# Kernel optimization log

Hardware: AMD Instinct MI355X
Metric: run time of the kernel (lower is better)

The kernel has to match this reference:

```python
import jax, jax.numpy as jnp
import numpy as np

R, C, N, E, H, F, ED, G, L = 1, 4, 50000, 200000, 128, 128, 16, 64, 2


def setup_inputs() -> dict:
    key = jax.random.key(0)
    ks = jax.random.split(key, 16)
    s = 0.05
    return {
        "x": jax.random.normal(ks[0], (R * C * N, H), jnp.float32),
        "batch": jnp.sort(jax.random.randint(ks[1], (N,), 0, G)),
        "edge_index": jax.random.randint(ks[2], (2, E), 0, N),
        "edge_attr": jax.random.normal(ks[3], (1, 1, E, ED), jnp.float32),
        "node_mask": jax.random.uniform(ks[4], (R, C, N, 1), jnp.float32),
        "edge_mask": jax.random.uniform(ks[5], (R, C, E, 1), jnp.float32),
        "W_be": jax.random.normal(ks[6], (ED, H), jnp.float32) * s,
        "b_be": jnp.zeros((H,), jnp.float32),
        "eps": jnp.zeros((L,), jnp.float32),
        "W1": jax.random.normal(ks[7], (L, H, H), jnp.float32) * s,
        "b1": jnp.zeros((L, H), jnp.float32),
        "W2": jax.random.normal(ks[8], (L, H, H), jnp.float32) * s,
        "b2": jnp.zeros((L, H), jnp.float32),
        "Wm1": jax.random.normal(ks[9], (H, H), jnp.float32) * s,
        "bm1": jnp.zeros((H,), jnp.float32),
        "Wm2": jax.random.normal(ks[10], (H, F), jnp.float32) * s,
        "bm2": jnp.zeros((F,), jnp.float32),
    }


def reference(x, batch, edge_index, edge_attr, node_mask, edge_mask,
              W_be, b_be, eps, W1, b1, W2, b2, Wm1, bm1, Wm2, bm2):
    gelu = lambda v: jax.nn.gelu(v, approximate=False)  # torch F.gelu default is erf
    src, dst = edge_index[0], edge_index[1]
    # bond encoder, shared across conv layers: (1,1,E,H)
    ee = edge_attr @ W_be + b_be
    for l in range(L):
        ux = x.reshape(R, C, N, H)
        # gather + add + GELU + edge-weight multiply: (R,C,E,H)
        msg = gelu(ux[:, :, src, :] + ee) * edge_mask
        # scatter_sum over edges into destination nodes
        agg = jnp.zeros_like(ux).at[:, :, dst, :].add(msg)
        h = (1.0 + eps[l]) * x + agg.reshape(x.shape)
        # conv MLP: Linear -> GELU -> Linear, then outer GELU (norm=Identity, dropout=0)
        h = gelu(h @ W1[l] + b1[l]) @ W2[l] + b2[l]
        x = gelu(h)
    # final node MLP (PyG MLP, norm=None): Linear -> GELU -> Linear
    x = gelu(x @ Wm1 + bm1) @ Wm2 + bm2  # (R*C*N, F)
    x4 = x.reshape(R, C, N, F)
    # masked mean-pool per (repeat, centroid, graph)
    num = jnp.zeros((R, C, G, F), x.dtype).at[:, :, batch, :].add(x4 * node_mask)
    den = jnp.zeros((R, C, G, 1), x.dtype).at[:, :, batch, :].add(node_mask) + 1e-7
    pooled = (num / den).transpose(0, 2, 1, 3).reshape(-1, F)  # (R*G*C, F)
    return pooled
```

## Files before the change

kernel.cpp:

```cpp
#include <hip/hip_runtime.h>
#include <math.h>

#define NN 50000
#define EN 200000
#define CC 4
#define HH 128
#define GG 64
#define LDSA 136
#define LDSF 132

typedef __attribute__((ext_vector_type(8))) short bs8;
typedef __attribute__((ext_vector_type(4))) float f32x4;
typedef __attribute__((ext_vector_type(2))) float f32x2;

__device__ __forceinline__ unsigned short f2bf(float f) {
  unsigned int u = __float_as_uint(f);
  u += 0x7FFFu + ((u >> 16) & 1u);
  return (unsigned short)(u >> 16);
}
__device__ __forceinline__ float bf2f(unsigned short h) {
  return __uint_as_float(((unsigned int)h) << 16);
}
__device__ __forceinline__ float gelu_f(float x) {
  float z = fabsf(x) * 0.7071067811865476f;
  float t = __builtin_amdgcn_rcpf(fmaf(0.3275911f, z, 1.0f));
  float poly = t * fmaf(t, fmaf(t, fmaf(t, fmaf(t, 1.061405429f, -1.453152027f),
                                        1.421413741f), -0.284496736f), 0.254829592f);
  float e = fmaf(-poly, __expf(-z * z), 1.0f);
  return 0.5f * x * (1.0f + copysignf(e, x));
}
__device__ __forceinline__ float gelu2_f(float x) {
  float z = fabsf(x) * 0.7071067811865476f;
  float t = __builtin_amdgcn_rcpf(fmaf(0.3275911f, z, 1.0f));
  float poly = t * fmaf(t, fmaf(t, fmaf(t, fmaf(t, 1.061405429f, -1.453152027f),
                                        1.421413741f), -0.284496736f), 0.254829592f);
  float e = fmaf(-poly, __expf(-z * z), 1.0f);
  return x * (1.0f + copysignf(e, x));
}

__global__ __launch_bounds__(256) void count_kernel(const int* __restrict__ dst,
                                                    int* __restrict__ counts) {
  int e = blockIdx.x * 256 + threadIdx.x;
  if (e < EN) atomicAdd(&counts[dst[e]], 1);
}

__global__ __launch_bounds__(256) void block_sum_kernel(const int* __restrict__ counts,
                                                        int* __restrict__ bsums) {
  int tid = threadIdx.x;
  int i = blockIdx.x * 256 + tid;
  int v = (i < NN) ? counts[i] : 0;
#pragma unroll
  for (int d = 1; d < 64; d <<= 1) v += __shfl_xor(v, d);
  __shared__ int ws4[4];
  if ((tid & 63) == 0) ws4[tid >> 6] = v;
  __syncthreads();
  if (tid == 0) bsums[blockIdx.x] = ws4[0] + ws4[1] + ws4[2] + ws4[3];
}

__global__ __launch_bounds__(256) void bsum_scan_kernel(const int* __restrict__ bsums,
                                                        int* __restrict__ boffs, int nb) {
  int tid = threadIdx.x, lane = tid & 63, wv = tid >> 6;
  int v = (tid < nb) ? bsums[tid] : 0;
  int s = v;
#pragma unroll
  for (int d = 1; d < 64; d <<= 1) { int t = __shfl_up(s, d); if (lane >= d) s += t; }
  __shared__ int wsum[4];
  if (lane == 63) wsum[wv] = s;
  __syncthreads();
  int pre = 0;
  for (int j = 0; j < wv; ++j) pre += wsum[j];
  if (tid < nb) boffs[tid] = pre + s - v;
}

__global__ __launch_bounds__(256) void block_scan_kernel(const int* __restrict__ counts,
                                                         const int* __restrict__ boffs,
                                                         int* __restrict__ offsets,
                                                         int* __restrict__ cursor) {
  int tid = threadIdx.x, lane = tid & 63, wv = tid >> 6;
  int i = blockIdx.x * 256 + tid;
  int v = (i < NN) ? counts[i] : 0;
  int s = v;
#pragma unroll
  for (int d = 1; d < 64; d <<= 1) { int t = __shfl_up(s, d); if (lane >= d) s += t; }
  __shared__ int wsum[4];
  if (lane == 63) wsum[wv] = s;
  __syncthreads();
  int pre = boffs[blockIdx.x];
  for (int j = 0; j < wv; ++j) pre += wsum[j];
  if (i < NN) { int e = pre + s - v; offsets[i] = e; cursor[i] = e; }
  if (i == 0) offsets[NN] = EN;
}

__global__ __launch_bounds__(256) void fill_kernel(const int* __restrict__ dst,
                                                   const int* __restrict__ src,
                                                   const float* __restrict__ emask,
                                                   int* __restrict__ cursor,
                                                   int2* __restrict__ csr_es,
                                                   float4* __restrict__ emask_s) {
  int e = blockIdx.x * 256 + threadIdx.x;
  if (e < EN) {
    int s = src[e];
    float m0 = emask[e];
    float m1 = emask[EN + e];
    float m2 = emask[2 * EN + e];
    float m3 = emask[3 * EN + e];
    int pos = atomicAdd(&cursor[dst[e]], 1);
    csr_es[pos] = make_int2(e, s);
    emask_s[pos] = make_float4(m0, m1, m2, m3);
  }
}

__global__ __launch_bounds__(256) void prep_w_kernel(const float* __restrict__ W1,
                                                     const float* __restrict__ W2,
                                                     const float* __restrict__ Wm1,
                                                     const float* __restrict__ Wm2,
                                                     unsigned short* __restrict__ wts) {
  int m = blockIdx.x >> 6;
  int idx = (blockIdx.x & 63) * 256 + threadIdx.x;
  const float* src = (m == 0) ? W1 : (m == 1) ? W1 + 16384 : (m == 2) ? W2
                     : (m == 3) ? W2 + 16384 : (m == 4) ? Wm1 : Wm2;
  unsigned short* dhi = wts + m * 32768;
  unsigned short* dlo = dhi + 16384;
  int n = idx >> 7, k = idx & 127;
  float v = src[k * HH + n];
  unsigned short hi = f2bf(v);
  dhi[n * HH + k] = hi;
  dlo[n * HH + k] = f2bf(v - bf2f(hi));
}

__global__ __launch_bounds__(256) void ee_kernel(const float* __restrict__ eattr,
                                                 const float* __restrict__ Wbe,
                                                 const float* __restrict__ bbe,
                                                 float* __restrict__ ee) {
  __shared__ float Ws[16 * HH];
  __shared__ float Ea[16 * 16];
  int tid = threadIdx.x;
  int e0 = blockIdx.x * 16;
#pragma unroll
  for (int i = 0; i < 8; ++i) Ws[tid + i * 256] = Wbe[tid + i * 256];
  Ea[tid] = eattr[(size_t)e0 * 16 + tid];
  __syncthreads();
  int h = tid & 127, half = tid >> 7;
  float bb = bbe[h];
#pragma unroll
  for (int j = 0; j < 8; ++j) {
    int el = j * 2 + half;
    float acc = bb;
#pragma unroll
    for (int d = 0; d < 16; ++d) acc += Ea[el * 16 + d] * Ws[d * HH + h];
    ee[(size_t)(e0 + el) * HH + h] = acc;
  }
}

__device__ __forceinline__ void loadW(const unsigned short* __restrict__ whi,
                                      const unsigned short* __restrict__ wlo,
                                      bs8 (&bh)[4][2], bs8 (&bl)[4][2],
                                      int ln, int quad, int wq) {
#pragma unroll
  for (int ks = 0; ks < 4; ++ks)
#pragma unroll
    for (int nt = 0; nt < 2; ++nt) {
      int wrow = ((wq * 2 + nt) * 16 + ln) * HH + ks * 32 + quad * 8;
      bh[ks][nt] = *(const bs8*)(whi + wrow);
      bl[ks][nt] = *(const bs8*)(wlo + wrow);
    }
}
__device__ __forceinline__ void zacc(f32x4 (&acc)[4][2]) {
#pragma unroll
  for (int mt = 0; mt < 4; ++mt)
#pragma unroll
    for (int nt = 0; nt < 2; ++nt)
#pragma unroll
      for (int r = 0; r < 4; ++r) acc[mt][nt][r] = 0.f;
}
__device__ __forceinline__ void gemm3(const unsigned short* Ahi, const unsigned short* Alo,
                                      const bs8 (&bh)[4][2], const bs8 (&bl)[4][2],
                                      f32x4 (&acc)[4][2], int ln, int quad) {
#pragma unroll
  for (int ks = 0; ks < 4; ++ks) {
    bs8 ah[4], al[4];
    int sb = ((ks * 4 + quad) ^ ln) * 8;
#pragma unroll
    for (int mt = 0; mt < 4; ++mt) {
      ah[mt] = *(const bs8*)(Ahi + (mt * 16 + ln) * HH + sb);
      al[mt] = *(const bs8*)(Alo + (mt * 16 + ln) * HH + sb);
    }
#pragma unroll
    for (int nt = 0; nt < 2; ++nt)
#pragma unroll
      for (int mt = 0; mt < 4; ++mt) {
        acc[mt][nt] = __builtin_amdgcn_mfma_f32_16x16x32_bf16(al[mt], bh[ks][nt], acc[mt][nt], 0, 0, 0);
        acc[mt][nt] = __builtin_amdgcn_mfma_f32_16x16x32_bf16(ah[mt], bl[ks][nt], acc[mt][nt], 0, 0, 0);
        acc[mt][nt] = __builtin_amdgcn_mfma_f32_16x16x32_bf16(ah[mt], bh[ks][nt], acc[mt][nt], 0, 0, 0);
      }
  }
}
__device__ __forceinline__ void tstage(unsigned short* Ahi, unsigned short* Alo,
                                       const float* __restrict__ b1v, f32x4 (&acc)[4][2],
                                       int ln, int quad, int wq) {
#pragma unroll
  for (int nt = 0; nt < 2; ++nt) {
    int col = (wq * 2 + nt) * 16 + ln;
    int cb = col >> 3, co = col & 7;
    float bb = b1v[col];
#pragma unroll
    for (int mt = 0; mt < 4; ++mt)
#pragma unroll
      for (int r = 0; r < 4; ++r) {
        float tv = gelu_f(acc[mt][nt][r] + bb);
        unsigned short th = f2bf(tv);
        int rr = mt * 16 + quad * 4 + r;
        int sof = rr * HH + (cb ^ (rr & 15)) * 8 + co;
        Ahi[sof] = th;
        Alo[sof] = f2bf(tv - bf2f(th));
      }
  }
}

__global__ __launch_bounds__(256, 4) void layer_kernel(
    const float* __restrict__ x,
    const float* __restrict__ ee,
    const int* __restrict__ off,
    const int2* __restrict__ csr_es,
    const float4* __restrict__ emask_s,
    const float* __restrict__ epsp, int layer,
    const unsigned short* __restrict__ w1hi, const unsigned short* __restrict__ w1lo,
    const float* __restrict__ b1,
    const unsigned short* __restrict__ w2hi, const unsigned short* __restrict__ w2lo,
    const float* __restrict__ b2,
    float* __restrict__ out) {
  __shared__ __align__(16) unsigned short AB[2 * 64 * HH];
  unsigned short* Ahi = AB;
  unsigned short* Alo = AB + 64 * HH;
  int tid = threadIdx.x;
  int lane = tid & 63, wq = tid >> 6;
  int ln = lane & 15, quad = lane >> 4;
  int n0 = blockIdx.x * 16;
  int c2 = lane * 2;
  float ep = 1.0f + epsp[layer];
  int blk = lane >> 2;
  int wo = (lane & 3) * 2;

  for (int j = 0; j < 4; ++j) {
    int nn = wq * 4 + j;
    int v = n0 + nn;
    float2 acc[CC];
#pragma unroll
    for (int c = 0; c < CC; ++c) { acc[c].x = 0.f; acc[c].y = 0.f; }
    int beg = off[v], end = off[v + 1];

    float2 eeC; float2 xC[CC]; float emC[CC];
    int2 esN = make_int2(0, 0);
    eeC.x = 0.f; eeC.y = 0.f;
#pragma unroll
    for (int c = 0; c < CC; ++c) { xC[c].x = 0.f; xC[c].y = 0.f; emC[c] = 0.f; }

    if (beg < end) {
      int2 es0 = csr_es[beg];
      eeC = *(const float2*)(ee + (size_t)es0.x * HH + c2);
#pragma unroll
      for (int c = 0; c < CC; ++c)
        xC[c] = *(const float2*)(x + ((size_t)c * NN + es0.y) * HH + c2);
      float4 m = emask_s[beg];
      emC[0] = 0.5f * m.x; emC[1] = 0.5f * m.y; emC[2] = 0.5f * m.z; emC[3] = 0.5f * m.w;
      if (beg + 1 < end) esN = csr_es[beg + 1];
    }

    for (int t = beg; t < end; ++t) {
      float2 eeB; float2 xB[CC]; float emB[CC];
      int2 esNN = make_int2(0, 0);
      if (t + 1 < end) {
        eeB = *(const float2*)(ee + (size_t)esN.x * HH + c2);
#pragma unroll
        for (int c = 0; c < CC; ++c)
          xB[c] = *(const float2*)(x + ((size_t)c * NN + esN.y) * HH + c2);
        float4 m = emask_s[t + 1];
        emB[0] = 0.5f * m.x; emB[1] = 0.5f * m.y; emB[2] = 0.5f * m.z; emB[3] = 0.5f * m.w;
        if (t + 2 < end) esNN = csr_es[t + 2];
      } else {
        eeB.x = 0.f; eeB.y = 0.f;
#pragma unroll
        for (int c = 0; c < CC; ++c) { xB[c].x = 0.f; xB[c].y = 0.f; emB[c] = 0.f; }
      }
#pragma unroll
      for (int c = 0; c < CC; ++c) {
        acc[c].x += gelu2_f(xC[c].x + eeC.x) * emC[c];
        acc[c].y += gelu2_f(xC[c].y + eeC.y) * emC[c];
      }
      eeC = eeB;
#pragma unroll
      for (int c = 0; c < CC; ++c) { xC[c] = xB[c]; emC[c] = emB[c]; }
      esN = esNN;
    }

#pragma unroll
    for (int c = 0; c < CC; ++c) {
      float2 xs = *(const float2*)(x + ((size_t)c * NN + v) * HH + c2);
      float o0 = fmaf(ep, xs.x, acc[c].x);
      float o1 = fmaf(ep, xs.y, acc[c].y);
      int rr = c * 16 + nn;
      int base = rr * HH + ((blk ^ (rr & 15)) * 8) + wo;
      unsigned short h0 = f2bf(o0), h1 = f2bf(o1);
      ushort2 hv; hv.x = h0; hv.y = h1;
      ushort2 lv; lv.x = f2bf(o0 - bf2f(h0)); lv.y = f2bf(o1 - bf2f(h1));
      *(ushort2*)(Ahi + base) = hv;
      *(ushort2*)(Alo + base) = lv;
    }
  }

  bs8 w1h[4][2], w1l[4][2];
  loadW(w1hi, w1lo, w1h, w1l, ln, quad, wq);
  __syncthreads();

  f32x4 acc[4][2];
  zacc(acc);
  gemm3(Ahi, Alo, w1h, w1l, acc, ln, quad);
  __syncthreads();

  bs8 w2h[4][2], w2l[4][2];
  loadW(w2hi, w2lo, w2h, w2l, ln, quad, wq);
  tstage(Ahi, Alo, b1, acc, ln, quad, wq);
  __syncthreads();

  zacc(acc);
  gemm3(Ahi, Alo, w2h, w2l, acc, ln, quad);

#pragma unroll
  for (int nt = 0; nt < 2; ++nt) {
    int col = (wq * 2 + nt) * 16 + ln;
    float bb = b2[col];
#pragma unroll
    for (int mt = 0; mt < 4; ++mt)
#pragma unroll
      for (int r = 0; r < 4; ++r) {
        float o = gelu_f(acc[mt][nt][r] + bb);
        out[((size_t)mt * NN + n0 + quad * 4 + r) * HH + col] = o;
      }
  }
}

__global__ __launch_bounds__(256, 2) void mlp_pool_kernel(
    const float* __restrict__ in,
    const unsigned short* __restrict__ w1hi, const unsigned short* __restrict__ w1lo,
    const float* __restrict__ b1,
    const unsigned short* __restrict__ w2hi, const unsigned short* __restrict__ w2lo,
    const float* __restrict__ b2,
    const float* __restrict__ nmask, const int* __restrict__ batch,
    float* __restrict__ num) {
  __shared__ __align__(16) unsigned short AB[128 * LDSA];
  __shared__ int kk[64];
  unsigned short* Ahi = AB;
  unsigned short* Alo = AB + 64 * LDSA;
  int tid = threadIdx.x;
  int row0 = blockIdx.x * 64;
  int lane = tid & 63, wq = tid >> 6;
  int ln = lane & 15, quad = lane >> 4;

  bs8 b1h[4][2], b1l[4][2];
  loadW(w1hi, w1lo, b1h, b1l, ln, quad, wq);
#pragma unroll
  for (int i = 0; i < 8; ++i) {
    int idx = tid + i * 256;
    int r = idx >> 5, cc4 = idx & 31;
    f32x4 vv = __builtin_nontemporal_load(
        (const f32x4*)(in + (size_t)(row0 + r) * HH + cc4 * 4));
    unsigned short h0 = f2bf(vv[0]), h1 = f2bf(vv[1]), h2 = f2bf(vv[2]), h3 = f2bf(vv[3]);
    ushort4 hv; hv.x = h0; hv.y = h1; hv.z = h2; hv.w = h3;
    ushort4 lv;
    lv.x = f2bf(vv[0] - bf2f(h0)); lv.y = f2bf(vv[1] - bf2f(h1));
    lv.z = f2bf(vv[2] - bf2f(h2)); lv.w = f2bf(vv[3] - bf2f(h3));
    *(ushort4*)(Ahi + r * LDSA + cc4 * 4) = hv;
    *(ushort4*)(Alo + r * LDSA + cc4 * 4) = lv;
  }
  if (tid < 64) {
    int gr = row0 + tid;
    int c = gr / NN;
    int n = gr - c * NN;
    kk[tid] = (c << 6) | batch[n];
  }
  __syncthreads();

  f32x4 acc[4][2];
  zacc(acc);
#pragma unroll
  for (int ks = 0; ks < 4; ++ks) {
    bs8 ah[4], al[4];
#pragma unroll
    for (int mt = 0; mt < 4; ++mt) {
      ah[mt] = *(const bs8*)(Ahi + (mt * 16 + ln) * LDSA + ks * 32 + quad * 8);
      al[mt] = *(const bs8*)(Alo + (mt * 16 + ln) * LDSA + ks * 32 + quad * 8);
    }
#pragma unroll
    for (int nt = 0; nt < 2; ++nt)
#pragma unroll
      for (int mt = 0; mt < 4; ++mt) {
        acc[mt][nt] = __builtin_amdgcn_mfma_f32_16x16x32_bf16(al[mt], b1h[ks][nt], acc[mt][nt], 0, 0, 0);
        acc[mt][nt] = __builtin_amdgcn_mfma_f32_16x16x32_bf16(ah[mt], b1l[ks][nt], acc[mt][nt], 0, 0, 0);
        acc[mt][nt] = __builtin_amdgcn_mfma_f32_16x16x32_bf16(ah[mt], b1h[ks][nt], acc[mt][nt], 0, 0, 0);
      }
  }
  __syncthreads();

  bs8 b2h[4][2], b2l[4][2];
  loadW(w2hi, w2lo, b2h, b2l, ln, quad, wq);
#pragma unroll
  for (int nt = 0; nt < 2; ++nt) {
    int col = (wq * 2 + nt) * 16 + ln;
    float bb = b1[col];
#pragma unroll
    for (int mt = 0; mt < 4; ++mt)
#pragma unroll
      for (int r = 0; r < 4; ++r) {
        float tv = gelu_f(acc[mt][nt][r] + bb);
        unsigned short th = f2bf(tv);
        int rr = mt * 16 + quad * 4 + r;
        Ahi[rr * LDSA + col] = th;
        Alo[rr * LDSA + col] = f2bf(tv - bf2f(th));
      }
  }
  __syncthreads();

  zacc(acc);
#pragma unroll
  for (int ks = 0; ks < 4; ++ks) {
    bs8 ah[4], al[4];
#pragma unroll
    for (int mt = 0; mt < 4; ++mt) {
      ah[mt] = *(const bs8*)(Ahi + (mt * 16 + ln) * LDSA + ks * 32 + quad * 8);
      al[mt] = *(const bs8*)(Alo + (mt * 16 + ln) * LDSA + ks * 32 + quad * 8);
    }
#pragma unroll
    for (int nt = 0; nt < 2; ++nt)
#pragma unroll
      for (int mt = 0; mt < 4; ++mt) {
        acc[mt][nt] = __builtin_amdgcn_mfma_f32_16x16x32_bf16(al[mt], b2h[ks][nt], acc[mt][nt], 0, 0, 0);
        acc[mt][nt] = __builtin_amdgcn_mfma_f32_16x16x32_bf16(ah[mt], b2l[ks][nt], acc[mt][nt], 0, 0, 0);
        acc[mt][nt] = __builtin_amdgcn_mfma_f32_16x16x32_bf16(ah[mt], b2h[ks][nt], acc[mt][nt], 0, 0, 0);
      }
  }
  __syncthreads();
  float* Tf = (float*)AB;
#pragma unroll
  for (int nt = 0; nt < 2; ++nt) {
    int col = (wq * 2 + nt) * 16 + ln;
    float bb = b2[col];
#pragma unroll
    for (int mt = 0; mt < 4; ++mt)
#pragma unroll
      for (int r = 0; r < 4; ++r) {
        int rl = mt * 16 + quad * 4 + r;
        int gr = row0 + rl;
        Tf[rl * LDSF + col] = (acc[mt][nt][r] + bb) * nmask[gr];
      }
  }
  __syncthreads();
  if (tid < 128) {
    int col = tid;
    float a2 = 0.f;
    int cur = kk[0];
    for (int r = 0; r < 64; ++r) {
      int k2 = kk[r];
      if (k2 != cur) {
        atomicAdd(&num[((size_t)(cur & 63) * CC + (cur >> 6)) * HH + col], a2);
        a2 = 0.f;
        cur = k2;
      }
      a2 += Tf[r * LDSF + col];
    }
    atomicAdd(&num[((size_t)(cur & 63) * CC + (cur >> 6)) * HH + col], a2);
  }
}

__global__ __launch_bounds__(256) void pool_finalize_kernel(const float* __restrict__ num,
                                                            const int* __restrict__ batch,
                                                            const float* __restrict__ nmask,
                                                            float* __restrict__ outp) {
  int g = blockIdx.x >> 2, c = blockIdx.x & 3;
  int lo = 0, hi = NN;
  while (lo < hi) { int m = (lo + hi) >> 1; if (batch[m] < g) lo = m + 1; else hi = m; }
  int start = lo;
  hi = NN;
  while (lo < hi) { int m = (lo + hi) >> 1; if (batch[m] < g + 1) lo = m + 1; else hi = m; }
  int end = lo;
  int tid = threadIdx.x;
  float d = 0.f;
  for (int n = start + tid; n < end; n += 256) d += nmask[c * NN + n];
#pragma unroll
  for (int k = 1; k < 64; k <<= 1) d += __shfl_xor(d, k);
  __shared__ float ws4[4];
  if ((tid & 63) == 0) ws4[tid >> 6] = d;
  __syncthreads();
  float den = ws4[0] + ws4[1] + ws4[2] + ws4[3] + 1e-7f;
  if (tid < 128) {
    int idx = blockIdx.x * 128 + tid;
    outp[idx] = num[idx] / den;
  }
}

extern "C" void kernel_launch(void* const* d_in, const int* in_sizes, int n_in,
                              void* d_out, int out_size, void* d_ws, size_t ws_size,
                              hipStream_t stream) {
  const float* x_in  = (const float*)d_in[0];
  const int*   batch = (const int*)d_in[1];
  const int*   eidx  = (const int*)d_in[2];
  const float* eattr = (const float*)d_in[3];
  const float* nmask = (const float*)d_in[4];
  const float* emask = (const float*)d_in[5];
  const float* Wbe   = (const float*)d_in[6];
  const float* bbe   = (const float*)d_in[7];
  const float* epsp  = (const float*)d_in[8];
  const float* W1    = (const float*)d_in[9];
  const float* b1    = (const float*)d_in[10];
  const float* W2    = (const float*)d_in[11];
  const float* b2    = (const float*)d_in[12];
  const float* Wm1   = (const float*)d_in[13];
  const float* bm1   = (const float*)d_in[14];
  const float* Wm2   = (const float*)d_in[15];
  const float* bm2   = (const float*)d_in[16];
  float* outp = (float*)d_out;

  const int* srcp = eidx;
  const int* dstp = eidx + EN;

  char* ws = (char*)d_ws;
  float* ee   = (float*)(ws);
  float* hbuf = (float*)(ws + 102400000);
  float* xbuf = (float*)(ws + 204800000);
  int* counts  = (int*)(ws + 307200000);
  int* offsets = (int*)(ws + 307400000);
  int* cursor  = (int*)(ws + 307600008);
  int2* csr_es = (int2*)(ws + 307800016);
  float4* emask_s = (float4*)(ws + 309400016);
  unsigned short* wts = (unsigned short*)(ws + 312600016);
  int* bsums = (int*)ws;
  int* boffs = (int*)(ws + 1024);
  float* num = (float*)ws;

  const int NB = (NN + 255) / 256;

  hipMemsetAsync(counts, 0, NN * sizeof(int), stream);
  count_kernel<<<(EN + 255) / 256, 256, 0, stream>>>(dstp, counts);
  block_sum_kernel<<<NB, 256, 0, stream>>>(counts, bsums);
  bsum_scan_kernel<<<1, 256, 0, stream>>>(bsums, boffs, NB);
  block_scan_kernel<<<NB, 256, 0, stream>>>(counts, boffs, offsets, cursor);
  fill_kernel<<<(EN + 255) / 256, 256, 0, stream>>>(dstp, srcp, emask, cursor, csr_es, emask_s);

  prep_w_kernel<<<384, 256, 0, stream>>>(W1, W2, Wm1, Wm2, wts);

  ee_kernel<<<EN / 16, 256, 0, stream>>>(eattr, Wbe, bbe, ee);

  layer_kernel<<<NN / 16, 256, 0, stream>>>(x_in, ee, offsets, csr_es, emask_s, epsp, 0,
                                            wts + 0, wts + 16384, b1,
                                            wts + 65536, wts + 81920, b2, hbuf);
  layer_kernel<<<NN / 16, 256, 0, stream>>>(hbuf, ee, offsets, csr_es, emask_s, epsp, 1,
                                            wts + 32768, wts + 49152, b1 + 128,
                                            wts + 98304, wts + 114688, b2 + 128, xbuf);
  hipMemsetAsync(num, 0, 131072, stream);
  mlp_pool_kernel<<<(CC * NN) / 64, 256, 0, stream>>>(xbuf, wts + 131072, wts + 147456, bm1,
                                                      wts + 163840, wts + 180224, bm2,
                                                      nmask, batch, num);
  pool_finalize_kernel<<<GG * CC, 256, 0, stream>>>(num, batch, nmask, outp);
}
```

Measured before the change: 678.5 us.

## Fuse bond encoder into layer kernel, recomputing edge embeddings from sorted edge_attr

Drops the separate ee_kernel, which wrote a 200000x128 fp32 edge-embedding buffer that both layers then gathered. The fill kernel now writes edge_attr (16 floats per edge) in CSR order, and each layer recomputes its two embedding columns per edge with 16 FMAs against Wbe held in registers. This removes the ~100 MB write and the repeated gathers of that buffer, and makes the edge reads contiguous. In exchange the layer kernels do extra ALU work and use more registers, which may reduce occupancy.

```diff
diff --git a/kernel.cpp b/kernel.cpp
--- a/kernel.cpp
+++ b/kernel.cpp
@@ -94,9 +94,11 @@
 __global__ __launch_bounds__(256) void fill_kernel(const int* __restrict__ dst,
                                                    const int* __restrict__ src,
                                                    const float* __restrict__ emask,
+                                                   const float* __restrict__ eattr,
                                                    int* __restrict__ cursor,
-                                                   int2* __restrict__ csr_es,
-                                                   float4* __restrict__ emask_s) {
+                                                   int* __restrict__ csr_s,
+                                                   float4* __restrict__ emask_s,
+                                                   float4* __restrict__ eattr_s) {
   int e = blockIdx.x * 256 + threadIdx.x;
   if (e < EN) {
     int s = src[e];
@@ -104,9 +106,15 @@
     float m1 = emask[EN + e];
     float m2 = emask[2 * EN + e];
     float m3 = emask[3 * EN + e];
+    const float4* ea = (const float4*)(eattr + (size_t)e * 16);
+    float4 a0 = ea[0], a1 = ea[1], a2 = ea[2], a3 = ea[3];
     int pos = atomicAdd(&cursor[dst[e]], 1);
-    csr_es[pos] = make_int2(e, s);
+    csr_s[pos] = s;
     emask_s[pos] = make_float4(m0, m1, m2, m3);
+    eattr_s[(size_t)pos * 4 + 0] = a0;
+    eattr_s[(size_t)pos * 4 + 1] = a1;
+    eattr_s[(size_t)pos * 4 + 2] = a2;
+    eattr_s[(size_t)pos * 4 + 3] = a3;
   }
 }
 
@@ -128,30 +136,6 @@
   dlo[n * HH + k] = f2bf(v - bf2f(hi));
 }
 
-__global__ __launch_bounds__(256) void ee_kernel(const float* __restrict__ eattr,
-                                                 const float* __restrict__ Wbe,
-                                                 const float* __restrict__ bbe,
-                                                 float* __restrict__ ee) {
-  __shared__ float Ws[16 * HH];
-  __shared__ float Ea[16 * 16];
-  int tid = threadIdx.x;
-  int e0 = blockIdx.x * 16;
-#pragma unroll
-  for (int i = 0; i < 8; ++i) Ws[tid + i * 256] = Wbe[tid + i * 256];
-  Ea[tid] = eattr[(size_t)e0 * 16 + tid];
-  __syncthreads();
-  int h = tid & 127, half = tid >> 7;
-  float bb = bbe[h];
-#pragma unroll
-  for (int j = 0; j < 8; ++j) {
-    int el = j * 2 + half;
-    float acc = bb;
-#pragma unroll
-    for (int d = 0; d < 16; ++d) acc += Ea[el * 16 + d] * Ws[d * HH + h];
-    ee[(size_t)(e0 + el) * HH + h] = acc;
-  }
-}
-
 __device__ __forceinline__ void loadW(const unsigned short* __restrict__ whi,
                                       const unsigned short* __restrict__ wlo,
                                       bs8 (&bh)[4][2], bs8 (&bl)[4][2],
@@ -196,13 +180,13 @@
   }
 }
 __device__ __forceinline__ void tstage(unsigned short* Ahi, unsigned short* Alo,
-                                       const float* __restrict__ b1v, f32x4 (&acc)[4][2],
+                                       const float* __restrict__ bv, f32x4 (&acc)[4][2],
                                        int ln, int quad, int wq) {
 #pragma unroll
   for (int nt = 0; nt < 2; ++nt) {
     int col = (wq * 2 + nt) * 16 + ln;
     int cb = col >> 3, co = col & 7;
-    float bb = b1v[col];
+    float bb = bv[col];
 #pragma unroll
     for (int mt = 0; mt < 4; ++mt)
 #pragma unroll
@@ -217,12 +201,121 @@
   }
 }
 
+__device__ __forceinline__ float2 ee_from_ea(const f32x4& a0, const f32x4& a1,
+                                             const f32x4& a2, const f32x4& a3,
+                                             const float (&w0a)[16], const float (&w1a)[16],
+                                             float bb0, float bb1) {
+  float e0 = bb0, e1 = bb1;
+#pragma unroll
+  for (int d = 0; d < 4; ++d) { e0 = fmaf(a0[d], w0a[d], e0);      e1 = fmaf(a0[d], w1a[d], e1); }
+#pragma unroll
+  for (int d = 0; d < 4; ++d) { e0 = fmaf(a1[d], w0a[4 + d], e0);  e1 = fmaf(a1[d], w1a[4 + d], e1); }
+#pragma unroll
+  for (int d = 0; d < 4; ++d) { e0 = fmaf(a2[d], w0a[8 + d], e0);  e1 = fmaf(a2[d], w1a[8 + d], e1); }
+#pragma unroll
+  for (int d = 0; d < 4; ++d) { e0 = fmaf(a3[d], w0a[12 + d], e0); e1 = fmaf(a3[d], w1a[12 + d], e1); }
+  return make_float2(e0, e1);
+}
+
+__device__ __forceinline__ void agg_phase(const float* __restrict__ x,
+                                          const float* __restrict__ eattr_s,
+                                          const int* __restrict__ off,
+                                          const int* __restrict__ csr_s,
+                                          const float4* __restrict__ emask_s,
+                                          const float* __restrict__ Wbe,
+                                          const float* __restrict__ bbe,
+                                          float ep, int n0,
+                                          unsigned short* Ahi, unsigned short* Alo,
+                                          int lane, int wq) {
+  int c2 = lane * 2;
+  int blk = lane >> 2;
+  int wo = (lane & 3) * 2;
+  float w0a[16], w1a[16];
+#pragma unroll
+  for (int d = 0; d < 16; ++d) {
+    float2 wv = *(const float2*)(Wbe + d * HH + c2);
+    w0a[d] = wv.x; w1a[d] = wv.y;
+  }
+  float2 bbv = *(const float2*)(bbe + c2);
+  float bb0 = bbv.x, bb1 = bbv.y;
+
+  for (int j = 0; j < 4; ++j) {
+    int nn = wq * 4 + j;
+    int v = n0 + nn;
+    float2 acc[CC];
+#pragma unroll
+    for (int c = 0; c < CC; ++c) { acc[c].x = 0.f; acc[c].y = 0.f; }
+    int beg = off[v], end = off[v + 1];
+
+    float2 eeC; float2 xC[CC]; float emC[CC]; int sN = 0;
+    eeC.x = 0.f; eeC.y = 0.f;
+#pragma unroll
+    for (int c = 0; c < CC; ++c) { xC[c].x = 0.f; xC[c].y = 0.f; emC[c] = 0.f; }
+
+    if (beg < end) {
+      int s0 = csr_s[beg];
+      const f32x4* ear = (const f32x4*)(eattr_s + (size_t)beg * 16);
+      f32x4 a0 = ear[0], a1 = ear[1], a2 = ear[2], a3 = ear[3];
+#pragma unroll
+      for (int c = 0; c < CC; ++c)
+        xC[c] = *(const float2*)(x + ((size_t)c * NN + s0) * HH + c2);
+      float4 m = emask_s[beg];
+      emC[0] = 0.5f * m.x; emC[1] = 0.5f * m.y; emC[2] = 0.5f * m.z; emC[3] = 0.5f * m.w;
+      eeC = ee_from_ea(a0, a1, a2, a3, w0a, w1a, bb0, bb1);
+      if (beg + 1 < end) sN = csr_s[beg + 1];
+    }
+
+    for (int t = beg; t < end; ++t) {
+      float2 xB[CC]; float emB[CC]; int sNN = 0;
+      f32x4 a0 = 0.f, a1 = 0.f, a2 = 0.f, a3 = 0.f;
+      bool has = (t + 1 < end);
+      if (has) {
+        const f32x4* ear = (const f32x4*)(eattr_s + (size_t)(t + 1) * 16);
+        a0 = ear[0]; a1 = ear[1]; a2 = ear[2]; a3 = ear[3];
+#pragma unroll
+        for (int c = 0; c < CC; ++c)
+          xB[c] = *(const float2*)(x + ((size_t)c * NN + sN) * HH + c2);
+        float4 m = emask_s[t + 1];
+        emB[0] = 0.5f * m.x; emB[1] = 0.5f * m.y; emB[2] = 0.5f * m.z; emB[3] = 0.5f * m.w;
+        if (t + 2 < end) sNN = csr_s[t + 2];
+      } else {
+#pragma unroll
+        for (int c = 0; c < CC; ++c) { xB[c].x = 0.f; xB[c].y = 0.f; emB[c] = 0.f; }
+      }
+#pragma unroll
+      for (int c = 0; c < CC; ++c) {
+        acc[c].x += gelu2_f(xC[c].x + eeC.x) * emC[c];
+        acc[c].y += gelu2_f(xC[c].y + eeC.y) * emC[c];
+      }
+      eeC = ee_from_ea(a0, a1, a2, a3, w0a, w1a, bb0, bb1);
+#pragma unroll
+      for (int c = 0; c < CC; ++c) { xC[c] = xB[c]; emC[c] = emB[c]; }
+      sN = sNN;
+    }
+
+#pragma unroll
+    for (int c = 0; c < CC; ++c) {
+      float2 xs = *(const float2*)(x + ((size_t)c * NN + v) * HH + c2);
+      float o0 = fmaf(ep, xs.x, acc[c].x);
+      float o1 = fmaf(ep, xs.y, acc[c].y);
+      int rr = c * 16 + nn;
+      int base = rr * HH + ((blk ^ (rr & 15)) * 8) + wo;
+      unsigned short h0 = f2bf(o0), h1 = f2bf(o1);
+      ushort2 hv; hv.x = h0; hv.y = h1;
+      ushort2 lv; lv.x = f2bf(o0 - bf2f(h0)); lv.y = f2bf(o1 - bf2f(h1));
+      *(ushort2*)(Ahi + base) = hv;
+      *(ushort2*)(Alo + base) = lv;
+    }
+  }
+}
+
 __global__ __launch_bounds__(256, 4) void layer_kernel(
     const float* __restrict__ x,
-    const float* __restrict__ ee,
+    const float* __restrict__ eattr_s,
     const int* __restrict__ off,
-    const int2* __restrict__ csr_es,
+    const int* __restrict__ csr_s,
     const float4* __restrict__ emask_s,
+    const float* __restrict__ Wbe, const float* __restrict__ bbe,
     const float* __restrict__ epsp, int layer,
     const unsigned short* __restrict__ w1hi, const unsigned short* __restrict__ w1lo,
     const float* __restrict__ b1,
@@ -236,77 +329,9 @@
   int lane = tid & 63, wq = tid >> 6;
   int ln = lane & 15, quad = lane >> 4;
   int n0 = blockIdx.x * 16;
-  int c2 = lane * 2;
-  float ep = 1.0f + epsp[layer];
-  int blk = lane >> 2;
-  int wo = (lane & 3) * 2;
-
-  for (int j = 0; j < 4; ++j) {
-    int nn = wq * 4 + j;
-    int v = n0 + nn;
-    float2 acc[CC];
-#pragma unroll
-    for (int c = 0; c < CC; ++c) { acc[c].x = 0.f; acc[c].y = 0.f; }
-    int beg = off[v], end = off[v + 1];
-
-    float2 eeC; float2 xC[CC]; float emC[CC];
-    int2 esN = make_int2(0, 0);
-    eeC.x = 0.f; eeC.y = 0.f;
-#pragma unroll
-    for (int c = 0; c < CC; ++c) { xC[c].x = 0.f; xC[c].y = 0.f; emC[c] = 0.f; }
-
-    if (beg < end) {
-      int2 es0 = csr_es[beg];
-      eeC = *(const float2*)(ee + (size_t)es0.x * HH + c2);
-#pragma unroll
-      for (int c = 0; c < CC; ++c)
-        xC[c] = *(const float2*)(x + ((size_t)c * NN + es0.y) * HH + c2);
-      float4 m = emask_s[beg];
-      emC[0] = 0.5f * m.x; emC[1] = 0.5f * m.y; emC[2] = 0.5f * m.z; emC[3] = 0.5f * m.w;
-      if (beg + 1 < end) esN = csr_es[beg + 1];
-    }
-
-    for (int t = beg; t < end; ++t) {
-      float2 eeB; float2 xB[CC]; float emB[CC];
-      int2 esNN = make_int2(0, 0);
-      if (t + 1 < end) {
-        eeB = *(const float2*)(ee + (size_t)esN.x * HH + c2);
-#pragma unroll
-        for (int c = 0; c < CC; ++c)
-          xB[c] = *(const float2*)(x + ((size_t)c * NN + esN.y) * HH + c2);
-        float4 m = emask_s[t + 1];
-        emB[0] = 0.5f * m.x; emB[1] = 0.5f * m.y; emB[2] = 0.5f * m.z; emB[3] = 0.5f * m.w;
-        if (t + 2 < end) esNN = csr_es[t + 2];
-      } else {
-        eeB.x = 0.f; eeB.y = 0.f;
-#pragma unroll
-        for (int c = 0; c < CC; ++c) { xB[c].x = 0.f; xB[c].y = 0.f; emB[c] = 0.f; }
-      }
-#pragma unroll
-      for (int c = 0; c < CC; ++c) {
-        acc[c].x += gelu2_f(xC[c].x + eeC.x) * emC[c];
-        acc[c].y += gelu2_f(xC[c].y + eeC.y) * emC[c];
-      }
-      eeC = eeB;
-#pragma unroll
-      for (int c = 0; c < CC; ++c) { xC[c] = xB[c]; emC[c] = emB[c]; }
-      esN = esNN;
-    }
-
-#pragma unroll
-    for (int c = 0; c < CC; ++c) {
-      float2 xs = *(const float2*)(x + ((size_t)c * NN + v) * HH + c2);
-      float o0 = fmaf(ep, xs.x, acc[c].x);
-      float o1 = fmaf(ep, xs.y, acc[c].y);
-      int rr = c * 16 + nn;
-      int base = rr * HH + ((blk ^ (rr & 15)) * 8) + wo;
-      unsigned short h0 = f2bf(o0), h1 = f2bf(o1);
-      ushort2 hv; hv.x = h0; hv.y = h1;
-      ushort2 lv; lv.x = f2bf(o0 - bf2f(h0)); lv.y = f2bf(o1 - bf2f(h1));
-      *(ushort2*)(Ahi + base) = hv;
-      *(ushort2*)(Alo + base) = lv;
-    }
-  }
+
+  agg_phase(x, eattr_s, off, csr_s, emask_s, Wbe, bbe,
+            1.0f + epsp[layer], n0, Ahi, Alo, lane, wq);
 
   bs8 w1h[4][2], w1l[4][2];
   loadW(w1hi, w1lo, w1h, w1l, ln, quad, wq);
@@ -523,15 +548,15 @@
   const int* dstp = eidx + EN;
 
   char* ws = (char*)d_ws;
-  float* ee   = (float*)(ws);
-  float* hbuf = (float*)(ws + 102400000);
-  float* xbuf = (float*)(ws + 204800000);
-  int* counts  = (int*)(ws + 307200000);
-  int* offsets = (int*)(ws + 307400000);
-  int* cursor  = (int*)(ws + 307600008);
-  int2* csr_es = (int2*)(ws + 307800016);
-  float4* emask_s = (float4*)(ws + 309400016);
-  unsigned short* wts = (unsigned short*)(ws + 312600016);
+  float* hbuf = (float*)(ws);
+  float* xbuf = (float*)(ws + 102400000);
+  int* counts  = (int*)(ws + 204800000);
+  int* offsets = (int*)(ws + 205000000);
+  int* cursor  = (int*)(ws + 205200008);
+  int* csr_s   = (int*)(ws + 205400008);
+  float4* emask_s = (float4*)(ws + 206200016);
+  float4* eattr_s = (float4*)(ws + 209400016);
+  unsigned short* wts = (unsigned short*)(ws + 222200016);
   int* bsums = (int*)ws;
   int* boffs = (int*)(ws + 1024);
   float* num = (float*)ws;
@@ -543,16 +568,17 @@
   block_sum_kernel<<<NB, 256, 0, stream>>>(counts, bsums);
   bsum_scan_kernel<<<1, 256, 0, stream>>>(bsums, boffs, NB);
   block_scan_kernel<<<NB, 256, 0, stream>>>(counts, boffs, offsets, cursor);
-  fill_kernel<<<(EN + 255) / 256, 256, 0, stream>>>(dstp, srcp, emask, cursor, csr_es, emask_s);
+  fill_kernel<<<(EN + 255) / 256, 256, 0, stream>>>(dstp, srcp, emask, eattr,
+                                                    cursor, csr_s, emask_s, eattr_s);
 
   prep_w_kernel<<<384, 256, 0, stream>>>(W1, W2, Wm1, Wm2, wts);
 
-  ee_kernel<<<EN / 16, 256, 0, stream>>>(eattr, Wbe, bbe, ee);
-
-  layer_kernel<<<NN / 16, 256, 0, stream>>>(x_in, ee, offsets, csr_es, emask_s, epsp, 0,
+  layer_kernel<<<NN / 16, 256, 0, stream>>>(x_in, (const float*)eattr_s, offsets, csr_s,
+                                            emask_s, Wbe, bbe, epsp, 0,
                                             wts + 0, wts + 16384, b1,
                                             wts + 65536, wts + 81920, b2, hbuf);
-  layer_kernel<<<NN / 16, 256, 0, stream>>>(hbuf, ee, offsets, csr_es, emask_s, epsp, 1,
+  layer_kernel<<<NN / 16, 256, 0, stream>>>(hbuf, (const float*)eattr_s, offsets, csr_s,
+                                            emask_s, Wbe, bbe, epsp, 1,
                                             wts + 32768, wts + 49152, b1 + 128,
                                             wts + 98304, wts + 114688, b2 + 128, xbuf);
   hipMemsetAsync(num, 0, 131072, stream);
```

Measured after the change: 634.9 us. -6.4%, faster.
